# Performance work log

Hardware: AMD Instinct MI355X
Metric: run time of the kernel (lower is better)

The kernel has to match this reference:

```python
import jax, jax.numpy as jnp
import numpy as np

SIZE = 512
ATTN = 64      # per-head attention_size
OUT = 64       # per-head output_size
HEADS = 8

def setup_inputs() -> dict:
    key = jax.random.key(0)
    ks = jax.random.split(key, 7)
    s = 0.02
    return {
        "x":  jax.random.normal(ks[0], (4, 2048, SIZE), dtype=jnp.float32),
        "Wq": jax.random.normal(ks[1], (SIZE, ATTN * HEADS), dtype=jnp.float32) * s,
        "bq": jax.random.normal(ks[2], (ATTN * HEADS,), dtype=jnp.float32) * s,
        "Wk": jax.random.normal(ks[3], (SIZE, ATTN), dtype=jnp.float32) * s,  # shared key, no bias
        "Wv": jax.random.normal(ks[4], (SIZE, OUT * HEADS), dtype=jnp.float32) * s,
        "bv": jax.random.normal(ks[5], (OUT * HEADS,), dtype=jnp.float32) * s,
    }

def reference(x, Wq, bq, Wk, Wv, bv):
    B, S, _ = x.shape
    q = (x @ Wq + bq).reshape(B, S, HEADS, ATTN)   # (B,S,H,A)
    k = x @ Wk                                      # (B,S,A) shared across heads
    v = (x @ Wv + bv).reshape(B, S, HEADS, OUT)     # (B,S,H,O)
    # NOTE: original divides by sqrt(seq_len), not sqrt(head_dim)
    scale = 1.0 / np.sqrt(S).astype(np.float32)
    scores = jnp.einsum("bqha,bka->bhqk", q, k) * scale  # (B,H,S,S)
    causal = jnp.tril(jnp.ones((S, S), dtype=bool))
    scores = jnp.where(causal, scores, -jnp.inf)
    attn = jax.nn.softmax(scores, axis=-1)
    out = jnp.einsum("bhqk,bkho->bqho", attn, v)    # (B,S,H,O)
    return out.reshape(B, S, HEADS * OUT)
```

## Files before the change

### kernel.cpp

```cpp
#include <hip/hip_runtime.h>
#include <math.h>


typedef _Float16 half8 __attribute__((ext_vector_type(8)));
typedef _Float16 half4 __attribute__((ext_vector_type(4)));
typedef float float4v __attribute__((ext_vector_type(4)));
typedef unsigned int u32;

#define SCL2E 0.031885926f

__device__ inline float4v mfma16(half8 a, half8 b, float4v c) {
    return __builtin_amdgcn_mfma_f32_16x16x32_f16(a, b, c, 0, 0, 0);
}
__device__ inline void load16(const _Float16* g, _Float16* l) {
    __builtin_amdgcn_global_load_lds((const __attribute__((address_space(1))) u32*)g,
                                     (__attribute__((address_space(3))) u32*)l, 16, 0, 0);
}

__global__ __launch_bounds__(256) void prep(
    const float* __restrict__ x, const float* __restrict__ Wq,
    const float* __restrict__ Wk, const float* __restrict__ Wv,
    _Float16* __restrict__ xh, _Float16* __restrict__ wqt,
    _Float16* __restrict__ wkt, _Float16* __restrict__ wvt) {
    const int bid = blockIdx.x;
    if (bid < 2048) {
        size_t base = (size_t)bid * 2048 + (size_t)threadIdx.x * 8;
        const float4* xp = (const float4*)(x + base);
        float4 f0 = xp[0], f1 = xp[1];
        half8 h = {(_Float16)f0.x, (_Float16)f0.y, (_Float16)f0.z, (_Float16)f0.w,
                   (_Float16)f1.x, (_Float16)f1.y, (_Float16)f1.z, (_Float16)f1.w};
        *(half8*)(xh + base) = h;
    } else {
        int r = bid - 2048;
        const float* W; _Float16* WT; int N, bx, by;
        if (r < 256)      { W = Wq; WT = wqt; N = 512; bx = r & 15; by = r >> 4; }
        else if (r < 288) { r -= 256; W = Wk; WT = wkt; N = 64;  bx = r & 1;  by = r >> 1; }
        else              { r -= 288; W = Wv; WT = wvt; N = 512; bx = r & 15; by = r >> 4; }
        __shared__ float T[32][33];
        const int tx = threadIdx.x & 31, ty = threadIdx.x >> 5;
        const int n0 = bx * 32, k0 = by * 32;
#pragma unroll
        for (int i = 0; i < 4; ++i)
            T[ty + 8 * i][tx] = W[(size_t)(k0 + ty + 8 * i) * N + n0 + tx];
        __syncthreads();
#pragma unroll
        for (int i = 0; i < 4; ++i)
            WT[(size_t)(n0 + ty + 8 * i) * 512 + k0 + tx] = (_Float16)T[tx][ty + 8 * i];
    }
}

__global__ __launch_bounds__(256) void qkv_gemm(
    const _Float16* __restrict__ xh,
    const _Float16* __restrict__ wqt, const _Float16* __restrict__ wkt,
    const _Float16* __restrict__ wvt,
    const float* __restrict__ bq, const float* __restrict__ bv,
    _Float16* __restrict__ q_ws, _Float16* __restrict__ kt_ws, _Float16* __restrict__ vt_ws) {
    __shared__ __align__(16) _Float16 Xs[8192];
    __shared__ __align__(16) _Float16 Ws[4096];

    const int m0 = blockIdx.x * 128;
    const int nt = blockIdx.y;
    const _Float16* WT;
    const float* bias;
    if (nt < 8)       { WT = wqt + (size_t)nt * 64 * 512; bias = bq + nt * 64; }
    else if (nt == 8) { WT = wkt;                          bias = nullptr; }
    else              { WT = wvt + (size_t)(nt - 9) * 64 * 512; bias = bv + (nt - 9) * 64; }

    const int tid = threadIdx.x;
    const int w = tid >> 6, lane = tid & 63, quad = lane >> 4, cl = lane & 15;
    const int lrow = lane >> 3;
    const int lgc = (lane & 7) ^ lrow;
    const _Float16* xg = xh + (size_t)(m0 + lrow) * 512 + lgc * 8;
    const _Float16* wg = WT + (size_t)lrow * 512 + lgc * 8;

    const int g0 = (quad ^ (cl & 7)) << 3;
    const int g1 = ((quad ^ 4) ^ (cl & 7)) << 3;

    float4v acc[2][4] = {};

    for (int ki = 0; ki < 8; ++ki) {
        const int kk = ki * 64;
        __syncthreads();
#pragma unroll
        for (int c = 0; c < 4; ++c) {
            int cc = w * 4 + c;
            load16(xg + (size_t)cc * 8 * 512 + kk, Xs + cc * 512);
        }
#pragma unroll
        for (int c = 0; c < 2; ++c) {
            int cc = w * 2 + c;
            load16(wg + (size_t)cc * 8 * 512 + kk, Ws + cc * 512);
        }
        __syncthreads();
#pragma unroll
        for (int c = 0; c < 2; ++c) {
            const int g = c ? g1 : g0;
#pragma unroll
            for (int s = 0; s < 2; ++s) {
                half8 a = *(const half8*)(Xs + (w * 32 + s * 16 + cl) * 64 + g);
#pragma unroll
                for (int j = 0; j < 4; ++j) {
                    half8 b = *(const half8*)(Ws + (j * 16 + cl) * 64 + g);
                    acc[s][j] = mfma16(a, b, acc[s][j]);
                }
            }
        }
    }

    if (nt < 8) {
#pragma unroll
        for (int s = 0; s < 2; ++s)
#pragma unroll
            for (int j = 0; j < 4; ++j)
#pragma unroll
                for (int r = 0; r < 4; ++r) {
                    int lr = w * 32 + s * 16 + quad * 4 + r;
                    int col = j * 16 + cl;
                    q_ws[(size_t)(m0 + lr) * 512 + nt * 64 + col] =
                        (_Float16)((acc[s][j][r] + bias[col]) * SCL2E);
                }
    } else if (nt == 8) {
#pragma unroll
        for (int s = 0; s < 2; ++s)
#pragma unroll
            for (int j = 0; j < 4; ++j)
#pragma unroll
                for (int r = 0; r < 4; ++r) {
                    int grow = m0 + w * 32 + s * 16 + quad * 4 + r;
                    int b = grow >> 11, t = (grow >> 6) & 31, row = grow & 63;
                    int col = j * 16 + cl;
                    kt_ws[((size_t)(b * 32 + t) << 12) + row * 64 +
                          (((col >> 3) ^ (row & 7)) << 3) + (col & 7)] = (_Float16)acc[s][j][r];
                }
    } else {
        const int h = nt - 9;
#pragma unroll
        for (int s = 0; s < 2; ++s)
#pragma unroll
            for (int j = 0; j < 4; ++j)
#pragma unroll
                for (int r = 0; r < 4; ++r) {
                    int grow = m0 + w * 32 + s * 16 + quad * 4 + r;
                    int b = grow >> 11, t = (grow >> 6) & 31, row = grow & 63;
                    int o = j * 16 + cl;
                    int kap = ((row & 15) << 2) + (row >> 4);
                    vt_ws[(((size_t)(b * 8 + h) * 32 + t) << 12) + o * 64 +
                          (((kap >> 3) ^ (o & 7)) << 3) + (kap & 7)] =
                        (_Float16)(acc[s][j][r] + bias[o]);
                }
    }
}

__global__ __launch_bounds__(256, 4) void attn(
    const _Float16* __restrict__ q_ws, const _Float16* __restrict__ kt_ws,
    const _Float16* __restrict__ vt_ws, float* __restrict__ out) {
    __shared__ __align__(16) _Float16 Ks[4096];
    __shared__ __align__(16) _Float16 VTs[2][4096];
    __shared__ __align__(16) _Float16 Ps[4][1024];

    const int bh = blockIdx.x, b = bh >> 3, h = bh & 7;
    const int y = blockIdx.y;
    int qt, half;
    if (y < 8)       { qt = 15 - y; half = 1; }
    else if (y < 16) { qt = y - 8;  half = 1; }
    else if (y < 24) { qt = 31 - y; half = 0; }
    else             { qt = y - 24; half = 0; }
    const int tlast = 2 * qt + half;
    const int q0 = qt * 128 + half * 64;

    const int bS = b * 2048;
    const int tid = threadIdx.x;
    const int w = tid >> 6, lane = tid & 63, quad = lane >> 4, cl = lane & 15;

    const _Float16* kbase = kt_ws + ((size_t)(b * 32) << 12);
    const _Float16* vbase = vt_ws + ((size_t)((b * 8 + h) * 32) << 12);

    const int g0 = (quad ^ (cl & 7)) << 3;
    const int g1 = ((quad ^ 4) ^ (cl & 7)) << 3;
    const int so0 = w * 1024 + lane * 8;

    const _Float16* qbase = q_ws + (size_t)(bS + q0 + w * 16 + cl) * 512 + h * 64;
    half8 qa0 = *(const half8*)(qbase + quad * 8);
    half8 qa1 = *(const half8*)(qbase + 32 + quad * 8);

    float4v oacc[4] = {};
    float l_run[4] = {0.f, 0.f, 0.f, 0.f};

    load16(kbase + so0,       &Ks[w * 1024]);
    load16(kbase + so0 + 512, &Ks[w * 1024 + 512]);
    load16(vbase + so0,       &VTs[0][w * 1024]);
    load16(vbase + so0 + 512, &VTs[0][w * 1024 + 512]);

    for (int t = 0; t <= tlast; ++t) {
        __syncthreads();
        if (t < tlast) {
            const _Float16* vt = vbase + ((size_t)(t + 1) << 12);
            load16(vt + so0,       &VTs[(t + 1) & 1][w * 1024]);
            load16(vt + so0 + 512, &VTs[(t + 1) & 1][w * 1024 + 512]);
        }
        const int ww = (t == tlast) ? w : 100;
        const int jmax = ww < 3 ? ww : 3;
        float4v sfr[4];
#pragma unroll
        for (int j = 0; j < 4; ++j) {
            if (j <= jmax) {
                const _Float16* kr = &Ks[(j * 16 + cl) * 64];
                half8 b0 = *(const half8*)(kr + g0);
                half8 b1 = *(const half8*)(kr + g1);
                float4v a_ = {0.f, 0.f, 0.f, 0.f};
                a_ = mfma16(qa0, b0, a_);
                a_ = mfma16(qa1, b1, a_);
                sfr[j] = a_;
            }
        }
#pragma unroll
        for (int r = 0; r < 4; ++r) {
            float pj[4];
#pragma unroll
            for (int j = 0; j < 4; ++j) {
                bool live = (j < jmax) || (j == jmax && (ww > 3 || cl <= quad * 4 + r));
                pj[j] = live ? exp2f(sfr[j][r]) : 0.f;
            }
            l_run[r] += (pj[0] + pj[1]) + (pj[2] + pj[3]);
            int rr = quad * 4 + r;
            half4 ph = {(_Float16)pj[0], (_Float16)pj[1], (_Float16)pj[2], (_Float16)pj[3]};
            *(half4*)&Ps[w][rr * 64 + ((((cl >> 1) ^ (rr & 7)) << 3) | ((cl & 1) << 2))] = ph;
        }
        __syncthreads();
        if (t < tlast) {
            const _Float16* kt = kbase + ((size_t)(t + 1) << 12);
            load16(kt + so0,       &Ks[w * 1024]);
            load16(kt + so0 + 512, &Ks[w * 1024 + 512]);
        }
        const _Float16* PB = &Ps[w][cl * 64];
        half8 pa0 = *(const half8*)(PB + g0);
        half8 pa1 = *(const half8*)(PB + g1);
        const int bb = t & 1;
#pragma unroll
        for (int jo = 0; jo < 4; ++jo) {
            const _Float16* vr = &VTs[bb][(jo * 16 + cl) * 64];
            half8 v0 = *(const half8*)(vr + g0);
            half8 v1 = *(const half8*)(vr + g1);
            oacc[jo] = mfma16(pa0, v0, oacc[jo]);
            oacc[jo] = mfma16(pa1, v1, oacc[jo]);
        }
    }
#pragma unroll
    for (int r = 0; r < 4; ++r) {
        float l = l_run[r];
        l += __shfl_xor(l, 1);
        l += __shfl_xor(l, 2);
        l += __shfl_xor(l, 4);
        l += __shfl_xor(l, 8);
        float inv = 1.0f / l;
        int row = q0 + w * 16 + quad * 4 + r;
        float* op = out + (size_t)(bS + row) * 512 + h * 64 + cl;
        op[0]  = oacc[0][r] * inv;
        op[16] = oacc[1][r] * inv;
        op[32] = oacc[2][r] * inv;
        op[48] = oacc[3][r] * inv;
    }
}

extern "C" void kernel_launch(void* const* d_in, const int* in_sizes, int n_in,
                              void* d_out, int out_size, void* d_ws, size_t ws_size,
                              hipStream_t stream) {
    const float* x  = (const float*)d_in[0];
    const float* Wq = (const float*)d_in[1];
    const float* bq = (const float*)d_in[2];
    const float* Wk = (const float*)d_in[3];
    const float* Wv = (const float*)d_in[4];
    const float* bv = (const float*)d_in[5];
    float* out = (float*)d_out;

    char* ws = (char*)d_ws;
    _Float16* q_ws  = (_Float16*)(ws);
    _Float16* kt_ws = (_Float16*)(ws + 8388608);
    _Float16* vt_ws = (_Float16*)(ws + 9437184);
    _Float16* wqt   = (_Float16*)(ws + 17825792);
    _Float16* wkt   = (_Float16*)(ws + 18350080);
    _Float16* wvt   = (_Float16*)(ws + 18415616);
    _Float16* xh    = (_Float16*)(ws + 18939904);

    prep<<<dim3(2592), dim3(256), 0, stream>>>(x, Wq, Wk, Wv, xh, wqt, wkt, wvt);

    qkv_gemm<<<dim3(64, 17), dim3(256), 0, stream>>>(
        xh, wqt, wkt, wvt, bq, bv, q_ws, kt_ws, vt_ws);

    attn<<<dim3(32, 32), dim3(256), 0, stream>>>(q_ws, kt_ws, vt_ws, out);
}
```

Baseline: 144.9 us.

## Double-buffer LDS tiles in QKV GEMM and K tiles in attention

The QKV projection GEMM now ping-pongs between two LDS buffers for the X and W tiles. It prefetches the next K-slice while running MFMAs on the current one, which drops one barrier per iteration. The attention kernel also double-buffers K tiles, so K and V for the next step are issued together at the top of the loop, and the mid-loop barrier before the K reload is gone. This aims to hide global-to-LDS latency behind MFMA work, at the cost of twice the LDS for these buffers, which could reduce occupancy.

```diff
diff --git a/kernel.cpp b/kernel.cpp
--- a/kernel.cpp
+++ b/kernel.cpp
@@ -55,8 +55,8 @@
     const _Float16* __restrict__ wvt,
     const float* __restrict__ bq, const float* __restrict__ bv,
     _Float16* __restrict__ q_ws, _Float16* __restrict__ kt_ws, _Float16* __restrict__ vt_ws) {
-    __shared__ __align__(16) _Float16 Xs[8192];
-    __shared__ __align__(16) _Float16 Ws[4096];
+    __shared__ __align__(16) _Float16 Xs[2][8192];
+    __shared__ __align__(16) _Float16 Ws[2][4096];
 
     const int m0 = blockIdx.x * 128;
     const int nt = blockIdx.y;
@@ -78,29 +78,42 @@
 
     float4v acc[2][4] = {};
 
+#pragma unroll
+    for (int c = 0; c < 4; ++c) {
+        int cc = w * 4 + c;
+        load16(xg + (size_t)cc * 8 * 512, Xs[0] + cc * 512);
+    }
+#pragma unroll
+    for (int c = 0; c < 2; ++c) {
+        int cc = w * 2 + c;
+        load16(wg + (size_t)cc * 8 * 512, Ws[0] + cc * 512);
+    }
+
     for (int ki = 0; ki < 8; ++ki) {
-        const int kk = ki * 64;
+        const int cb = ki & 1, nb = cb ^ 1;
         __syncthreads();
-#pragma unroll
-        for (int c = 0; c < 4; ++c) {
-            int cc = w * 4 + c;
-            load16(xg + (size_t)cc * 8 * 512 + kk, Xs + cc * 512);
-        }
-#pragma unroll
-        for (int c = 0; c < 2; ++c) {
-            int cc = w * 2 + c;
-            load16(wg + (size_t)cc * 8 * 512 + kk, Ws + cc * 512);
-        }
-        __syncthreads();
+        if (ki < 7) {
+            const int kk = (ki + 1) * 64;
+#pragma unroll
+            for (int c = 0; c < 4; ++c) {
+                int cc = w * 4 + c;
+                load16(xg + (size_t)cc * 8 * 512 + kk, Xs[nb] + cc * 512);
+            }
+#pragma unroll
+            for (int c = 0; c < 2; ++c) {
+                int cc = w * 2 + c;
+                load16(wg + (size_t)cc * 8 * 512 + kk, Ws[nb] + cc * 512);
+            }
+        }
 #pragma unroll
         for (int c = 0; c < 2; ++c) {
             const int g = c ? g1 : g0;
 #pragma unroll
             for (int s = 0; s < 2; ++s) {
-                half8 a = *(const half8*)(Xs + (w * 32 + s * 16 + cl) * 64 + g);
+                half8 a = *(const half8*)(Xs[cb] + (w * 32 + s * 16 + cl) * 64 + g);
 #pragma unroll
                 for (int j = 0; j < 4; ++j) {
-                    half8 b = *(const half8*)(Ws + (j * 16 + cl) * 64 + g);
+                    half8 b = *(const half8*)(Ws[cb] + (j * 16 + cl) * 64 + g);
                     acc[s][j] = mfma16(a, b, acc[s][j]);
                 }
             }
@@ -154,7 +167,7 @@
 __global__ __launch_bounds__(256, 4) void attn(
     const _Float16* __restrict__ q_ws, const _Float16* __restrict__ kt_ws,
     const _Float16* __restrict__ vt_ws, float* __restrict__ out) {
-    __shared__ __align__(16) _Float16 Ks[4096];
+    __shared__ __align__(16) _Float16 Ks[2][4096];
     __shared__ __align__(16) _Float16 VTs[2][4096];
     __shared__ __align__(16) _Float16 Ps[4][1024];
 
@@ -186,17 +199,21 @@
     float4v oacc[4] = {};
     float l_run[4] = {0.f, 0.f, 0.f, 0.f};
 
-    load16(kbase + so0,       &Ks[w * 1024]);
-    load16(kbase + so0 + 512, &Ks[w * 1024 + 512]);
+    load16(kbase + so0,       &Ks[0][w * 1024]);
+    load16(kbase + so0 + 512, &Ks[0][w * 1024 + 512]);
     load16(vbase + so0,       &VTs[0][w * 1024]);
     load16(vbase + so0 + 512, &VTs[0][w * 1024 + 512]);
 
     for (int t = 0; t <= tlast; ++t) {
+        const int cb = t & 1, nb = cb ^ 1;
         __syncthreads();
         if (t < tlast) {
+            const _Float16* kt = kbase + ((size_t)(t + 1) << 12);
             const _Float16* vt = vbase + ((size_t)(t + 1) << 12);
-            load16(vt + so0,       &VTs[(t + 1) & 1][w * 1024]);
-            load16(vt + so0 + 512, &VTs[(t + 1) & 1][w * 1024 + 512]);
+            load16(kt + so0,       &Ks[nb][w * 1024]);
+            load16(kt + so0 + 512, &Ks[nb][w * 1024 + 512]);
+            load16(vt + so0,       &VTs[nb][w * 1024]);
+            load16(vt + so0 + 512, &VTs[nb][w * 1024 + 512]);
         }
         const int ww = (t == tlast) ? w : 100;
         const int jmax = ww < 3 ? ww : 3;
@@ -204,7 +221,7 @@
 #pragma unroll
         for (int j = 0; j < 4; ++j) {
             if (j <= jmax) {
-                const _Float16* kr = &Ks[(j * 16 + cl) * 64];
+                const _Float16* kr = &Ks[cb][(j * 16 + cl) * 64];
                 half8 b0 = *(const half8*)(kr + g0);
                 half8 b1 = *(const half8*)(kr + g1);
                 float4v a_ = {0.f, 0.f, 0.f, 0.f};
@@ -226,19 +243,12 @@
             half4 ph = {(_Float16)pj[0], (_Float16)pj[1], (_Float16)pj[2], (_Float16)pj[3]};
             *(half4*)&Ps[w][rr * 64 + ((((cl >> 1) ^ (rr & 7)) << 3) | ((cl & 1) << 2))] = ph;
         }
-        __syncthreads();
-        if (t < tlast) {
-            const _Float16* kt = kbase + ((size_t)(t + 1) << 12);
-            load16(kt + so0,       &Ks[w * 1024]);
-            load16(kt + so0 + 512, &Ks[w * 1024 + 512]);
-        }
         const _Float16* PB = &Ps[w][cl * 64];
         half8 pa0 = *(const half8*)(PB + g0);
         half8 pa1 = *(const half8*)(PB + g1);
-        const int bb = t & 1;
 #pragma unroll
         for (int jo = 0; jo < 4; ++jo) {
-            const _Float16* vr = &VTs[bb][(jo * 16 + cl) * 64];
+            const _Float16* vr = &VTs[cb][(jo * 16 + cl) * 64];
             half8 v0 = *(const half8*)(vr + g0);
             half8 v1 = *(const half8*)(vr + g1);
             oacc[jo] = mfma16(pa0, v0, oacc[jo]);
```

Result: no change. 144.5 us (-0.3%).
